# Performance work log

Measured on AMD Instinct MI355X. Metric: run time of the kernel, lower is better.

Reference implementation:

```python
import jax, jax.numpy as jnp
import numpy as np

B, IN, H, Z = 2048, 1024, 1024, 256


def setup_inputs() -> dict:
    key = jax.random.key(0)
    ks = jax.random.split(key, 17)
    s = 1.0 / np.sqrt(H)  # matches reset_parameters uniform(-stdv, stdv)
    u = lambda k, shape: jax.random.uniform(k, shape, minval=-s, maxval=s, dtype=jnp.float32)
    return {
        'src_x': jax.random.normal(ks[0], (B, IN), dtype=jnp.float32),
        'h': jax.random.normal(ks[1], (B, H), dtype=jnp.float32),
        'c': jax.random.normal(ks[2], (B, H), dtype=jnp.float32),
        'src_meta': jax.random.normal(ks[3], (B, Z), dtype=jnp.float32),
        'zh_w': u(ks[4], (4 * Z, Z)),
        'zh_b': u(ks[5], (4 * Z,)),
        'zx_w': u(ks[6], (4 * Z, Z)),
        'zx_b': u(ks[7], (4 * Z,)),
        'zb_w': u(ks[8], (4 * Z, Z)),
        'dh_w': u(ks[9], (4, H, Z)),
        'dx_w': u(ks[10], (4, H, Z)),
        'db_w': u(ks[11], (4, H, Z)),
        'db_b': u(ks[12], (4, H)),
        'w_h': u(ks[13], (4, H, H)),
        'w_x': u(ks[14], (4, H, IN)),
        'ln_w': u(ks[15], (4, H)),
        'ln_b': u(ks[16], (4, H)),
    }


def reference(src_x, h, c, src_meta, zh_w, zh_b, zx_w, zx_b, zb_w,
              dh_w, dx_w, db_w, db_b, w_h, w_x, ln_w, ln_b):
    b = src_x.shape[0]
    # hypernetwork projections, reshaped to [B, 4 gates, Z]
    zh = (src_meta @ zh_w.T + zh_b).reshape(b, 4, -1)
    zx = (src_meta @ zx_w.T + zx_b).reshape(b, 4, -1)
    zb = (src_meta @ zb_w.T).reshape(b, 4, -1)
    # per-gate scaling vectors d_h, d_x and bias d_b: [B, 4, H]
    d_h = jnp.einsum('bgz,ghz->bgh', zh, dh_w)
    d_x = jnp.einsum('bgz,ghz->bgh', zx, dx_w)
    d_b = jnp.einsum('bgz,ghz->bgh', zb, db_w) + db_b[None]
    # main LSTM matmuls: [B, 4, H]
    wh = jnp.einsum('ghj,bj->bgh', w_h, h)
    wx = jnp.einsum('ghj,bj->bgh', w_x, src_x)
    y = d_h * wh + d_x * wx + d_b
    # per-gate LayerNorm over hidden dim (eps = 1e-5, torch default)
    mu = jnp.mean(y, axis=-1, keepdims=True)
    var = jnp.var(y, axis=-1, keepdims=True)
    yn = (y - mu) * jax.lax.rsqrt(var + 1e-5) * ln_w[None] + ln_b[None]
    i, f, g, o = yn[:, 0], yn[:, 1], yn[:, 2], yn[:, 3]
    c_next = jax.nn.sigmoid(f) * c + jax.nn.sigmoid(i) * jnp.tanh(g)
    h_next = jax.nn.sigmoid(o) * jnp.tanh(c_next)
    return (h_next, c_next)
```

## Files before the change

kernel.cpp:

```cpp
#include <hip/hip_runtime.h>

typedef __attribute__((ext_vector_type(4))) float f32x4;
typedef __attribute__((ext_vector_type(16))) float f32x16;
typedef __attribute__((ext_vector_type(8))) short bf16x8;

#define DEVFN static __device__ __forceinline__

DEVFN unsigned short f2bf(float f) {
  union { float f; unsigned u; } x; x.f = f;
  unsigned r = x.u + 0x7fffu + ((x.u >> 16) & 1u);
  return (unsigned short)(r >> 16);
}
DEVFN float bf2f(unsigned short u) {
  union { unsigned u; float f; } x; x.u = ((unsigned)u) << 16;
  return x.f;
}

DEVFN void gload_lds16(const unsigned short* g, unsigned short* l) {
  __builtin_amdgcn_global_load_lds(
      (const __attribute__((address_space(1))) unsigned int*)g,
      (__attribute__((address_space(3))) unsigned int*)l, 16, 0, 0);
}

#define NSEG 11
struct SegTable {
  const float* src[NSEG];
  unsigned short* dst[NSEG];
  int chunks[NSEG];
};

__global__ __launch_bounds__(256) void cast_f32_bf16(SegTable st) {
  int c = blockIdx.x;
  int s = 0;
  while (c >= st.chunks[s]) { c -= st.chunks[s]; ++s; }
  const float* src = st.src[s] + (long)c * 4096;
  unsigned short* dst = st.dst[s] + (long)c * 4096;
  const int t = threadIdx.x;
#pragma unroll
  for (int i = 0; i < 4; ++i) {
    float4 v = *(const float4*)(src + t * 4 + i * 1024);
    ushort4 o;
    o.x = f2bf(v.x); o.y = f2bf(v.y); o.z = f2bf(v.z); o.w = f2bf(v.w);
    *(ushort4*)(dst + t * 4 + i * 1024) = o;
  }
}

__global__ void build_zbias(const float* __restrict__ zh_b,
                            const float* __restrict__ zx_b,
                            float* __restrict__ out) {
  int i = blockIdx.x * 256 + threadIdx.x;
  float v = 0.f;
  if (i < 1024) v = zh_b[i];
  else if (i < 2048) v = zx_b[i - 1024];
  out[i] = v;
}

DEVFN void gemm128_body(const unsigned short* __restrict__ A,
                        const unsigned short* __restrict__ W,
                        unsigned short* __restrict__ C,
                        const float* __restrict__ bias,
                        int lda, int ldb, int ldc, int K,
                        int bx, int by,
                        unsigned short* As, unsigned short* Bs) {
  const int m0 = by * 128, n0 = bx * 128;
  const int tid = threadIdx.x;
  const int lane = tid & 63, wid = tid >> 6;
  const int wr = wid >> 1, wc = wid & 1;

  const int srow = tid >> 2, scol = (tid & 3) * 8;
  const unsigned short* Ag0 = A + (long)(m0 + srow) * lda + scol;
  const unsigned short* Ag1 = A + (long)(m0 + 64 + srow) * lda + scol;
  const unsigned short* Wg0 = W + (long)(n0 + srow) * ldb + scol;
  const unsigned short* Wg1 = W + (long)(n0 + 64 + srow) * ldb + scol;
  unsigned short* As0 = &As[tid * 8];
  unsigned short* As1 = &As[2048 + tid * 8];
  unsigned short* Bs0 = &Bs[tid * 8];
  unsigned short* Bs1 = &Bs[2048 + tid * 8];

  const int r = lane & 15, q = lane >> 4;

  f32x4 acc[4][4];
#pragma unroll
  for (int m = 0; m < 4; ++m)
#pragma unroll
    for (int n = 0; n < 4; ++n) acc[m][n] = (f32x4)0.f;

  for (int k0 = 0; k0 < K; k0 += 32) {
    gload_lds16(Ag0 + k0, As0);
    gload_lds16(Ag1 + k0, As1);
    gload_lds16(Wg0 + k0, Bs0);
    gload_lds16(Wg1 + k0, Bs1);
    __syncthreads();

    bf16x8 af[4], bfr[4];
#pragma unroll
    for (int m = 0; m < 4; ++m)
      af[m] = *(const bf16x8*)&As[(wr * 64 + m * 16 + r) * 32 + q * 8];
#pragma unroll
    for (int n = 0; n < 4; ++n)
      bfr[n] = *(const bf16x8*)&Bs[(wc * 64 + n * 16 + r) * 32 + q * 8];
#pragma unroll
    for (int m = 0; m < 4; ++m)
#pragma unroll
      for (int n = 0; n < 4; ++n)
        acc[m][n] = __builtin_amdgcn_mfma_f32_16x16x32_bf16(af[m], bfr[n],
                                                            acc[m][n], 0, 0, 0);
    __syncthreads();
  }

#pragma unroll
  for (int m = 0; m < 4; ++m) {
    const int row = m0 + wr * 64 + m * 16 + q * 4;
#pragma unroll
    for (int n = 0; n < 4; ++n) {
      const int col = n0 + wc * 64 + n * 16 + r;
      float bv = bias ? bias[col] : 0.f;
#pragma unroll
      for (int j = 0; j < 4; ++j) {
        float v = acc[m][n][j] + bv;
        C[(long)(row + j) * ldc + col] = f2bf(v);
      }
    }
  }
}

__global__ __launch_bounds__(256) void gemm_z(
    const unsigned short* __restrict__ A, const unsigned short* __restrict__ W,
    unsigned short* __restrict__ C, const float* __restrict__ bias) {
  __shared__ __align__(16) unsigned short As[128 * 32];
  __shared__ __align__(16) unsigned short Bs[128 * 32];
  gemm128_body(A, W, C, bias, 256, 256, 3072, 256, blockIdx.x, blockIdx.y, As, Bs);
}

__global__ __launch_bounds__(256) void gemm_d(
    const unsigned short* __restrict__ zcat, const unsigned short* __restrict__ Wd,
    unsigned short* __restrict__ dall, const float* __restrict__ db_b) {
  __shared__ __align__(16) unsigned short As[128 * 32];
  __shared__ __align__(16) unsigned short Bs[128 * 32];
  const int zz = blockIdx.z;
  const int t = zz >> 2, g = zz & 3;
  const unsigned short* A = zcat + t * 1024 + g * 256;
  const unsigned short* W = Wd + (long)zz * 262144;
  unsigned short* C = dall + (long)t * 8388608 + g * 1024;
  if (t == 2) {
    gemm128_body(A, W, C, db_b + g * 1024, 3072, 256, 4096, 256,
                 blockIdx.x, blockIdx.y, As, Bs);
  } else {
    gemm128_body(A, W, C, nullptr, 3072, 256, 4096, 256,
                 blockIdx.x, blockIdx.y, As, Bs);
  }
}

__global__ __launch_bounds__(512, 2) void gemm256_whx(
    const unsigned short* __restrict__ Aall,
    const unsigned short* __restrict__ Ball,
    unsigned short* __restrict__ Call) {
  __shared__ __align__(16) unsigned short As[2][2][8192];
  __shared__ __align__(16) unsigned short Bs[2][2][8192];

  const int bid = blockIdx.x;
  const int swz = (bid & 7) * 32 + (bid >> 3);
  const int z = swz >> 7;
  const int rr = swz & 127;
  const int sb = rr >> 5, wq = rr & 31;
  const int my = (sb & 1) * 4 + (wq >> 3);
  const int nx = (sb >> 1) * 8 + (wq & 7);

  const unsigned short* Ag = Aall + (long)z * 2097152 + (long)my * 262144;
  const unsigned short* Bg = Ball + (long)z * 4194304 + (long)nx * 262144;
  unsigned short* Cg = Call + (long)z * 8388608 + (long)my * 1048576 + nx * 256;

  const int tid = threadIdx.x;
  const int lane = tid & 63, wid = tid >> 6;
  const int wm = wid >> 2, wn = wid & 3;
  const int l31 = lane & 31, l5 = lane >> 5;
  const int sw = l31 & 7;

  const int srow = tid >> 3, sslot = tid & 7;
  const int gcol = (sslot ^ (srow & 7)) * 8;
  const unsigned short* AgS = Ag + (long)srow * 1024 + gcol;
  const unsigned short* BgS = Bg + (long)srow * 1024 + gcol;

  auto stageA = [&](int buf, int half, int kt) {
    const unsigned short* s = AgS + half * 131072 + kt * 64;
    unsigned short* d = &As[buf][half][tid * 8];
    gload_lds16(s, d);
    gload_lds16(s + 65536, d + 4096);
  };
  auto stageB = [&](int buf, int half, int kt) {
    const unsigned short* s = BgS + half * 131072 + kt * 64;
    unsigned short* d = &Bs[buf][half][tid * 8];
    gload_lds16(s, d);
    gload_lds16(s + 65536, d + 4096);
  };

  int koff[4];
#pragma unroll
  for (int ks = 0; ks < 4; ++ks) koff[ks] = ((ks * 2 + l5) ^ sw) * 8;

  const int bhalf = wn >> 1;
  int brow[2];
#pragma unroll
  for (int nt = 0; nt < 2; ++nt) brow[nt] = ((wn & 1) * 64 + nt * 32 + l31) * 64;
  int arow[4];
#pragma unroll
  for (int mt = 0; mt < 4; ++mt) arow[mt] = (mt * 32 + l31) * 64;

  f32x16 acc[4][2];
#pragma unroll
  for (int m = 0; m < 4; ++m)
#pragma unroll
    for (int n = 0; n < 2; ++n) acc[m][n] = (f32x16)0.f;

  stageA(0, 0, 0); stageB(0, 0, 0); stageA(0, 1, 0); stageB(0, 1, 0);
  stageA(1, 0, 1); stageB(1, 0, 1);
  asm volatile("s_waitcnt vmcnt(4)" ::: "memory");
  __builtin_amdgcn_s_barrier();

#pragma unroll 2
  for (int T = 0; T < 16; ++T) {
    const int buf = T & 1, nb = buf ^ 1;

    if (T < 15) { stageA(nb, 1, T + 1); stageB(nb, 1, T + 1); }

    bf16x8 bfg[2][4], af[2][4];
    const unsigned short* Ab = &As[buf][wm][0];
    {
      const unsigned short* Bb = &Bs[buf][bhalf][0];
#pragma unroll
      for (int nt = 0; nt < 2; ++nt)
#pragma unroll
        for (int ks = 0; ks < 4; ++ks)
          bfg[nt][ks] = *(const bf16x8*)(Bb + brow[nt] + koff[ks]);
#pragma unroll
      for (int m2 = 0; m2 < 2; ++m2)
#pragma unroll
        for (int ks = 0; ks < 4; ++ks)
          af[m2][ks] = *(const bf16x8*)(Ab + arow[m2] + koff[ks]);
    }

    __builtin_amdgcn_s_setprio(1);
#pragma unroll
    for (int m2 = 0; m2 < 2; ++m2)
#pragma unroll
      for (int nt = 0; nt < 2; ++nt)
#pragma unroll
        for (int ks = 0; ks < 4; ++ks)
          acc[m2][nt] = __builtin_amdgcn_mfma_f32_32x32x16_bf16(
              af[m2][ks], bfg[nt][ks], acc[m2][nt], 0, 0, 0);
    __builtin_amdgcn_s_setprio(0);

#pragma unroll
    for (int m2 = 0; m2 < 2; ++m2)
#pragma unroll
      for (int ks = 0; ks < 4; ++ks)
        af[m2][ks] = *(const bf16x8*)(Ab + arow[2 + m2] + koff[ks]);

    asm volatile("s_waitcnt lgkmcnt(0)" ::: "memory");
    __builtin_amdgcn_sched_barrier(0);
    __builtin_amdgcn_s_barrier();

    if (T < 14) { stageA(buf, 0, T + 2); stageB(buf, 0, T + 2); }

    __builtin_amdgcn_s_setprio(1);
#pragma unroll
    for (int m2 = 0; m2 < 2; ++m2)
#pragma unroll
      for (int nt = 0; nt < 2; ++nt)
#pragma unroll
        for (int ks = 0; ks < 4; ++ks)
          acc[2 + m2][nt] = __builtin_amdgcn_mfma_f32_32x32x16_bf16(
              af[m2][ks], bfg[nt][ks], acc[2 + m2][nt], 0, 0, 0);
    __builtin_amdgcn_s_setprio(0);

    if (T < 14) {
      asm volatile("s_waitcnt vmcnt(4)" ::: "memory");
      __builtin_amdgcn_s_barrier();
    } else if (T == 14) {
      asm volatile("s_waitcnt vmcnt(0)" ::: "memory");
      __builtin_amdgcn_s_barrier();
    }
  }

#pragma unroll
  for (int mt = 0; mt < 4; ++mt) {
#pragma unroll
    for (int nt = 0; nt < 2; ++nt) {
      const int rb = wm * 128 + mt * 32 + 4 * l5;
      const int cb = wn * 64 + nt * 32 + l31;
#pragma unroll
      for (int reg = 0; reg < 16; ++reg) {
        const int row = rb + (reg & 3) + 8 * (reg >> 2);
        Cg[(long)row * 4096 + cb] = f2bf(acc[mt][nt][reg]);
      }
    }
  }
}

DEVFN void ld4bf(const unsigned short* p, float* o) {
  ushort4 v = *(const ushort4*)p;
  o[0] = bf2f(v.x); o[1] = bf2f(v.y); o[2] = bf2f(v.z); o[3] = bf2f(v.w);
}

__global__ __launch_bounds__(256) void epilogue_kernel(
    const unsigned short* __restrict__ d_all,
    const unsigned short* __restrict__ whx,
    const float* __restrict__ c_in,
    const float* __restrict__ ln_w, const float* __restrict__ ln_b,
    float* __restrict__ out) {
  const long b = blockIdx.x;
  const int t = threadIdx.x;
  const int lane = t & 63, wid = t >> 6;

  const unsigned short* dh = d_all + b * 4096;
  const unsigned short* dx = d_all + 8388608L + b * 4096;
  const unsigned short* db = d_all + 16777216L + b * 4096;
  const unsigned short* wh = whx + b * 4096;
  const unsigned short* wx = whx + 8388608L + b * 4096;

  __shared__ float redS[4][4], redQ[4][4];
  float y[4][4];

#pragma unroll
  for (int g = 0; g < 4; ++g) {
    const int base = g * 1024 + t * 4;
    float fdh[4], fdx[4], fdb[4], fwh[4], fwx[4];
    ld4bf(dh + base, fdh);
    ld4bf(dx + base, fdx);
    ld4bf(db + base, fdb);
    ld4bf(wh + base, fwh);
    ld4bf(wx + base, fwx);
    float s = 0.f, sq = 0.f;
#pragma unroll
    for (int j = 0; j < 4; ++j) {
      float v = fdh[j] * fwh[j] + fdx[j] * fwx[j] + fdb[j];
      y[g][j] = v;
      s += v;
      sq += v * v;
    }
#pragma unroll
    for (int off = 32; off; off >>= 1) {
      s += __shfl_down(s, off);
      sq += __shfl_down(sq, off);
    }
    if (lane == 0) { redS[g][wid] = s; redQ[g][wid] = sq; }
  }
  __syncthreads();

  float yn[4][4];
#pragma unroll
  for (int g = 0; g < 4; ++g) {
    float S = redS[g][0] + redS[g][1] + redS[g][2] + redS[g][3];
    float SQ = redQ[g][0] + redQ[g][1] + redQ[g][2] + redQ[g][3];
    float mu = S * (1.f / 1024.f);
    float var = SQ * (1.f / 1024.f) - mu * mu;
    float rs = rsqrtf(var + 1e-5f);
    const int base = g * 1024 + t * 4;
    float4 lw = *(const float4*)(ln_w + base);
    float4 lb = *(const float4*)(ln_b + base);
    yn[g][0] = (y[g][0] - mu) * rs * lw.x + lb.x;
    yn[g][1] = (y[g][1] - mu) * rs * lw.y + lb.y;
    yn[g][2] = (y[g][2] - mu) * rs * lw.z + lb.z;
    yn[g][3] = (y[g][3] - mu) * rs * lw.w + lb.w;
  }

  float4 cp = *(const float4*)(c_in + b * 1024 + t * 4);
  float cin[4] = {cp.x, cp.y, cp.z, cp.w};
  float hn[4], cn[4];
#pragma unroll
  for (int j = 0; j < 4; ++j) {
    float ii = yn[0][j], ff = yn[1][j], gg = yn[2][j], oo = yn[3][j];
    float si = 1.f / (1.f + expf(-ii));
    float sf = 1.f / (1.f + expf(-ff));
    float so = 1.f / (1.f + expf(-oo));
    float cnj = sf * cin[j] + si * tanhf(gg);
    cn[j] = cnj;
    hn[j] = so * tanhf(cnj);
  }
  float4 ho = {hn[0], hn[1], hn[2], hn[3]};
  float4 co = {cn[0], cn[1], cn[2], cn[3]};
  *(float4*)(out + b * 1024 + t * 4) = ho;
  *(float4*)(out + 2097152L + b * 1024 + t * 4) = co;
}

extern "C" void kernel_launch(void* const* d_in, const int* in_sizes, int n_in,
                              void* d_out, int out_size, void* d_ws,
                              size_t ws_size, hipStream_t stream) {
  const float* src_x = (const float*)d_in[0];
  const float* h_in  = (const float*)d_in[1];
  const float* c_in  = (const float*)d_in[2];
  const float* meta  = (const float*)d_in[3];
  const float* zh_w  = (const float*)d_in[4];
  const float* zh_b  = (const float*)d_in[5];
  const float* zx_w  = (const float*)d_in[6];
  const float* zx_b  = (const float*)d_in[7];
  const float* zb_w  = (const float*)d_in[8];
  const float* dh_w  = (const float*)d_in[9];
  const float* dx_w  = (const float*)d_in[10];
  const float* db_w  = (const float*)d_in[11];
  const float* db_b  = (const float*)d_in[12];
  const float* w_h   = (const float*)d_in[13];
  const float* w_x   = (const float*)d_in[14];
  const float* ln_w  = (const float*)d_in[15];
  const float* ln_b  = (const float*)d_in[16];

  char* ws = (char*)d_ws;
  unsigned short* h_bf    = (unsigned short*)(ws + 0);
  unsigned short* x_bf    = (unsigned short*)(ws + 4194304);
  unsigned short* meta_bf = (unsigned short*)(ws + 8388608);
  unsigned short* Wh      = (unsigned short*)(ws + 9437184);
  unsigned short* Wx      = (unsigned short*)(ws + 17825792);
  unsigned short* Wz      = (unsigned short*)(ws + 26214400);
  unsigned short* Wd      = (unsigned short*)(ws + 27787264);
  unsigned short* zcat    = (unsigned short*)(ws + 34078720);
  unsigned short* dall    = (unsigned short*)(ws + 46661632);
  unsigned short* whx     = (unsigned short*)(ws + 96993280);
  float* zcat_b           = (float*)(ws + 130547712);
  if (ws_size < 130560000) return;

  SegTable st;
  int i = 0, total = 0;
  auto add = [&](const float* s, unsigned short* d, int n) {
    st.src[i] = s; st.dst[i] = d; st.chunks[i] = n / 4096;
    total += n / 4096; ++i;
  };
  add(h_in, h_bf, 2048 * 1024);
  add(src_x, x_bf, 2048 * 1024);
  add(meta, meta_bf, 2048 * 256);
  add(w_h, Wh, 4096 * 1024);
  add(w_x, Wx, 4096 * 1024);
  add(zh_w, Wz, 1024 * 256);
  add(zx_w, Wz + 262144, 1024 * 256);
  add(zb_w, Wz + 524288, 1024 * 256);
  add(dh_w, Wd, 4 * 1024 * 256);
  add(dx_w, Wd + 1048576, 4 * 1024 * 256);
  add(db_w, Wd + 2097152, 4 * 1024 * 256);
  cast_f32_bf16<<<total, 256, 0, stream>>>(st);
  build_zbias<<<12, 256, 0, stream>>>(zh_b, zx_b, zcat_b);

  gemm_z<<<dim3(24, 16, 1), 256, 0, stream>>>(meta_bf, Wz, zcat, zcat_b);

  gemm_d<<<dim3(8, 16, 12), 256, 0, stream>>>(zcat, Wd, dall, db_b);

  gemm256_whx<<<256, 512, 0, stream>>>(h_bf, Wh, whx);

  epilogue_kernel<<<2048, 256, 0, stream>>>(dall, whx, c_in, ln_w, ln_b,
                                            (float*)d_out);
}
```

Before: 122.5 us.

## Fold hypernetwork Z projection into D weights by precomposing the two linear maps

```diff
diff --git a/kernel.cpp b/kernel.cpp
--- a/kernel.cpp
+++ b/kernel.cpp
@@ -22,7 +22,7 @@
       (__attribute__((address_space(3))) unsigned int*)l, 16, 0, 0);
 }
 
-#define NSEG 11
+#define NSEG 8
 struct SegTable {
   const float* src[NSEG];
   unsigned short* dst[NSEG];
@@ -45,14 +45,59 @@
   }
 }
 
-__global__ void build_zbias(const float* __restrict__ zh_b,
-                            const float* __restrict__ zx_b,
-                            float* __restrict__ out) {
-  int i = blockIdx.x * 256 + threadIdx.x;
-  float v = 0.f;
-  if (i < 1024) v = zh_b[i];
-  else if (i < 2048) v = zx_b[i - 1024];
-  out[i] = v;
+__global__ __launch_bounds__(256) void tcast_z(
+    const float* __restrict__ zh_w, const float* __restrict__ zx_w,
+    const float* __restrict__ zb_w, unsigned short* __restrict__ WzT) {
+  const int zz = blockIdx.z;
+  const int t = zz >> 2, g = zz & 3;
+  const float* src =
+      (t == 0 ? zh_w : (t == 1 ? zx_w : zb_w)) + (long)g * 65536;
+  unsigned short* dst = WzT + (long)zz * 65536;
+  const int j0 = blockIdx.x * 64, k0 = blockIdx.y * 64;
+  __shared__ float T[64][65];
+  const int tid = threadIdx.x;
+  const int jr = tid >> 2, kc = (tid & 3) * 16;
+#pragma unroll
+  for (int i = 0; i < 4; ++i) {
+    float4 v = *(const float4*)(src + (long)(j0 + jr) * 256 + k0 + kc + i * 4);
+    T[jr][kc + i * 4 + 0] = v.x;
+    T[jr][kc + i * 4 + 1] = v.y;
+    T[jr][kc + i * 4 + 2] = v.z;
+    T[jr][kc + i * 4 + 3] = v.w;
+  }
+  __syncthreads();
+  const int kr = tid >> 2, jc = (tid & 3) * 16;
+  unsigned short tmp[16];
+#pragma unroll
+  for (int i = 0; i < 16; ++i) tmp[i] = f2bf(T[jc + i][kr]);
+  *(bf16x8*)(dst + (long)(k0 + kr) * 256 + j0 + jc) = *(bf16x8*)&tmp[0];
+  *(bf16x8*)(dst + (long)(k0 + kr) * 256 + j0 + jc + 8) = *(bf16x8*)&tmp[8];
+}
+
+__global__ __launch_bounds__(256) void fbias_kernel(
+    const float* __restrict__ zh_b, const float* __restrict__ zx_b,
+    const float* __restrict__ db_b, const float* __restrict__ dh_w,
+    const float* __restrict__ dx_w, float* __restrict__ F) {
+  if (blockIdx.x >= 128) {
+    const int idx = (blockIdx.x - 128) * 1024 + threadIdx.x * 4;
+    *(float4*)(F + 8192 + idx) = *(const float4*)(db_b + idx);
+    return;
+  }
+  const int wgid = blockIdx.x * 4 + (threadIdx.x >> 6);
+  const int lane = threadIdx.x & 63;
+  const int t = wgid >> 8, g = (wgid >> 6) & 3, hbase = (wgid & 63) * 16;
+  const float* zb = (t == 0 ? zh_b : zx_b) + g * 256;
+  const float* dw = (t == 0 ? dh_w : dx_w) + (long)g * 262144;
+  float4 zv = *(const float4*)(zb + lane * 4);
+#pragma unroll
+  for (int i = 0; i < 16; ++i) {
+    const int h = hbase + i;
+    float4 wv = *(const float4*)(dw + (long)h * 256 + lane * 4);
+    float s = zv.x * wv.x + zv.y * wv.y + zv.z * wv.z + zv.w * wv.w;
+#pragma unroll
+    for (int off = 32; off; off >>= 1) s += __shfl_down(s, off);
+    if (lane == 0) F[(t * 4 + g) * 1024 + h] = s;
+  }
 }
 
 DEVFN void gemm128_body(const unsigned short* __restrict__ A,
@@ -124,31 +169,26 @@
   }
 }
 
-__global__ __launch_bounds__(256) void gemm_z(
-    const unsigned short* __restrict__ A, const unsigned short* __restrict__ W,
-    unsigned short* __restrict__ C, const float* __restrict__ bias) {
-  __shared__ __align__(16) unsigned short As[128 * 32];
-  __shared__ __align__(16) unsigned short Bs[128 * 32];
-  gemm128_body(A, W, C, bias, 256, 256, 3072, 256, blockIdx.x, blockIdx.y, As, Bs);
+__global__ __launch_bounds__(256) void gemm_e(
+    const unsigned short* __restrict__ Wd, const unsigned short* __restrict__ WzT,
+    unsigned short* __restrict__ E) {
+  __shared__ __align__(16) unsigned short As[4096];
+  __shared__ __align__(16) unsigned short Bs[4096];
+  const int zz = blockIdx.z;
+  gemm128_body(Wd + (long)zz * 262144, WzT + (long)zz * 65536,
+               E + (long)zz * 262144, nullptr,
+               256, 256, 256, 256, blockIdx.x, blockIdx.y, As, Bs);
 }
 
 __global__ __launch_bounds__(256) void gemm_d(
-    const unsigned short* __restrict__ zcat, const unsigned short* __restrict__ Wd,
-    unsigned short* __restrict__ dall, const float* __restrict__ db_b) {
-  __shared__ __align__(16) unsigned short As[128 * 32];
-  __shared__ __align__(16) unsigned short Bs[128 * 32];
+    const unsigned short* __restrict__ meta_bf, const unsigned short* __restrict__ E,
+    unsigned short* __restrict__ dall, const float* __restrict__ F) {
+  __shared__ __align__(16) unsigned short As[4096];
+  __shared__ __align__(16) unsigned short Bs[4096];
   const int zz = blockIdx.z;
-  const int t = zz >> 2, g = zz & 3;
-  const unsigned short* A = zcat + t * 1024 + g * 256;
-  const unsigned short* W = Wd + (long)zz * 262144;
-  unsigned short* C = dall + (long)t * 8388608 + g * 1024;
-  if (t == 2) {
-    gemm128_body(A, W, C, db_b + g * 1024, 3072, 256, 4096, 256,
-                 blockIdx.x, blockIdx.y, As, Bs);
-  } else {
-    gemm128_body(A, W, C, nullptr, 3072, 256, 4096, 256,
-                 blockIdx.x, blockIdx.y, As, Bs);
-  }
+  unsigned short* C = dall + (long)(zz >> 2) * 8388608 + (zz & 3) * 1024;
+  gemm128_body(meta_bf, E + (long)zz * 262144, C, F + zz * 1024,
+               256, 256, 4096, 256, blockIdx.x, blockIdx.y, As, Bs);
 }
 
 __global__ __launch_bounds__(512, 2) void gemm256_whx(
@@ -410,13 +450,13 @@
   unsigned short* meta_bf = (unsigned short*)(ws + 8388608);
   unsigned short* Wh      = (unsigned short*)(ws + 9437184);
   unsigned short* Wx      = (unsigned short*)(ws + 17825792);
-  unsigned short* Wz      = (unsigned short*)(ws + 26214400);
-  unsigned short* Wd      = (unsigned short*)(ws + 27787264);
-  unsigned short* zcat    = (unsigned short*)(ws + 34078720);
-  unsigned short* dall    = (unsigned short*)(ws + 46661632);
-  unsigned short* whx     = (unsigned short*)(ws + 96993280);
-  float* zcat_b           = (float*)(ws + 130547712);
-  if (ws_size < 130560000) return;
+  unsigned short* Wd      = (unsigned short*)(ws + 26214400);
+  unsigned short* WzT     = (unsigned short*)(ws + 32505856);
+  unsigned short* E       = (unsigned short*)(ws + 34078720);
+  float*          F       = (float*)(ws + 40370176);
+  unsigned short* dall    = (unsigned short*)(ws + 40419328);
+  unsigned short* whx     = (unsigned short*)(ws + 90750976);
+  if (ws_size < 124305408) return;
 
   SegTable st;
   int i = 0, total = 0;
@@ -429,18 +469,17 @@
   add(meta, meta_bf, 2048 * 256);
   add(w_h, Wh, 4096 * 1024);
   add(w_x, Wx, 4096 * 1024);
-  add(zh_w, Wz, 1024 * 256);
-  add(zx_w, Wz + 262144, 1024 * 256);
-  add(zb_w, Wz + 524288, 1024 * 256);
   add(dh_w, Wd, 4 * 1024 * 256);
   add(dx_w, Wd + 1048576, 4 * 1024 * 256);
   add(db_w, Wd + 2097152, 4 * 1024 * 256);
   cast_f32_bf16<<<total, 256, 0, stream>>>(st);
-  build_zbias<<<12, 256, 0, stream>>>(zh_b, zx_b, zcat_b);
-
-  gemm_z<<<dim3(24, 16, 1), 256, 0, stream>>>(meta_bf, Wz, zcat, zcat_b);
-
-  gemm_d<<<dim3(8, 16, 12), 256, 0, stream>>>(zcat, Wd, dall, db_b);
+
+  tcast_z<<<dim3(4, 4, 12), 256, 0, stream>>>(zh_w, zx_w, zb_w, WzT);
+  fbias_kernel<<<132, 256, 0, stream>>>(zh_b, zx_b, db_b, dh_w, dx_w, F);
+
+  gemm_e<<<dim3(2, 8, 12), 256, 0, stream>>>(Wd, WzT, E);
+
+  gemm_d<<<dim3(8, 16, 12), 256, 0, stream>>>(meta_bf, E, dall, F);
 
   gemm256_whx<<<256, 512, 0, stream>>>(h_bf, Wh, whx);
 
```

Result: no change. 121.9 us (-0.4%).
